# Optimization experiments

Measured on AMD Instinct MI355X. Metric: run time of the kernel, lower is better.

The kernel has to match this reference:

```python
import jax, jax.numpy as jnp
import numpy as np

B, C_CONV, C_TRANS, L = 2048, 64, 64, 16
CT = C_CONV + C_TRANS            # 128 input channels
DIM = C_TRANS                    # transformer width (must equal trans_dim)
HEADS, DIM_HEAD = 8, 64          # Attention defaults
INNER = HEADS * DIM_HEAD         # 512
DEPTH, FF_HID = 2, 256           # Block1D -> Transformer defaults
WLEN = 4                         # Attention.lenth (hardcoded in source)
SCALE = DIM_HEAD ** -0.5

# static relative-position indices (16x16) from 4x4 coordinate grid
_cord = np.array([[i, j] for i in range(WLEN) for j in range(WLEN)])
_rel = _cord[:, None, :] - _cord[None, :, :] + WLEN - 1   # values in [0, 6]
_REL0, _REL1 = _rel[..., 0], _rel[..., 1]

def _build_sw_mask():
    h, w, p, shift = HEADS // 2, 2, WLEN, WLEN // 2
    m = np.zeros((h, w, p, p, p, p), dtype=bool)
    s = p - shift
    m[-1, :, :s, :, s:, :] = True
    m[-1, :, s:, :, :s, :] = True
    m[:, -1, :, :s, :, s:] = True
    m[:, -1, :, s:, :, :s] = True
    return jnp.asarray(m.reshape(1, h * w, p * p, p * p))  # (1, heads, 16, 16)

_MASK = _build_sw_mask()

def _ln(x, g, b, eps=1e-5):
    m = x.mean(-1, keepdims=True)
    v = ((x - m) ** 2).mean(-1, keepdims=True)
    return (x - m) / jnp.sqrt(v + eps) * g + b

def _conv1d(x, w, b, pad):
    y = jax.lax.conv_general_dilated(x, w, (1,), [(pad, pad)],
                                     dimension_numbers=('NCH', 'OIH', 'NCH'))
    return y + b[None, :, None]

def _attention(x, qkv_w, qkv_b, proj_w, proj_b, relpos):
    b, n, _ = x.shape
    x = jnp.roll(x, -(n // 2), axis=1)            # SW cyclic shift (never un-rolled, as in source)
    qkv = x @ qkv_w.T + qkv_b                     # (b, n, 3*inner)
    q, k, v = jnp.split(qkv, 3, axis=-1)
    sh = lambda t: t.reshape(b, n, HEADS, DIM_HEAD).transpose(0, 2, 1, 3)
    q, k, v = sh(q), sh(k), sh(v)
    dots = jnp.einsum('bhid,bhjd->bhij', q, k) * SCALE
    dots = dots + relpos[:, _REL0, _REL1][None]   # gathered relative-position bias (heads,n,n)
    dots = jnp.where(_MASK[:, :, :n, :n], -1e9, dots)
    attn = jax.nn.softmax(dots, axis=-1)
    out = jnp.einsum('bhij,bhjd->bhid', attn, v)
    out = out.transpose(0, 2, 1, 3).reshape(b, n, INNER)
    return out @ proj_w.T + proj_b

def _forward(x, c11_w, c11_b, c12_w, c12_b, lse1_w, lse1_b, lse2_w, lse2_b,
             ln1_g, ln1_b, ln2_g, ln2_b, mlp1_w, mlp1_b, mlp2_w, mlp2_b,
             aln_g, aln_b, qkv_w, qkv_b, proj_w, proj_b, relpos,
             fln_g, fln_b, ff1_w, ff1_b, ff2_w, ff2_b):
    y = jax.nn.relu(_conv1d(x, c11_w, c11_b, 0))
    conv_x, trans_x = y[:, :C_CONV], y[:, C_CONV:]
    # LSE residual block, plus the extra residual in VSE.forward
    t = jax.nn.leaky_relu(_conv1d(conv_x, lse1_w, lse1_b, 1), 0.01)
    t = jax.nn.leaky_relu(_conv1d(t, lse2_w, lse2_b, 1), 0.01)
    conv_x = (t + conv_x) + conv_x
    # GSE: Block1D(trans_dim, trans_dim, dim)
    h = trans_x.transpose(0, 2, 1)                # (b, l, c)
    z = _ln(h, ln1_g, ln1_b)
    for i in range(DEPTH):
        z = _attention(_ln(z, aln_g[i], aln_b[i]), qkv_w[i], qkv_b[i],
                       proj_w[i], proj_b[i], relpos[i]) + z
        f = _ln(z, fln_g[i], fln_b[i])
        f = jax.nn.gelu(f @ ff1_w[i].T + ff1_b[i], approximate=False)
        z = f @ ff2_w[i].T + ff2_b[i] + z
    h = h + z                                     # x + msa(ln1(x))
    m = _ln(h, ln2_g, ln2_b)
    m = jax.nn.gelu(m @ mlp1_w.T + mlp1_b, approximate=False)
    h = h + (m @ mlp2_w.T + mlp2_b)               # x + mlp(ln2(x))
    trans_out = h.transpose(0, 2, 1)              # (b, c, l)
    res = _conv1d(jnp.concatenate([conv_x, trans_out], axis=1), c12_w, c12_b, 0)
    return x + res

def setup_inputs() -> dict:
    key = jax.random.key(0)
    ks = iter(jax.random.split(key, 40))
    rnd = lambda shape, s=0.02: jax.random.normal(next(ks), shape, jnp.float32) * s
    return {
        'x': jax.random.normal(next(ks), (B, CT, L), jnp.float32),
        'c11_w': rnd((CT, CT, 1), 0.05), 'c11_b': rnd((CT,)),
        'c12_w': rnd((CT, CT, 1), 0.05), 'c12_b': rnd((CT,)),
        'lse1_w': rnd((C_CONV, C_CONV, 3), 0.05), 'lse1_b': rnd((C_CONV,)),
        'lse2_w': rnd((C_CONV, C_CONV, 3), 0.05), 'lse2_b': rnd((C_CONV,)),
        'ln1_g': jnp.ones((DIM,)), 'ln1_b': jnp.zeros((DIM,)),
        'ln2_g': jnp.ones((DIM,)), 'ln2_b': jnp.zeros((DIM,)),
        'mlp1_w': rnd((4 * DIM, DIM)), 'mlp1_b': rnd((4 * DIM,)),
        'mlp2_w': rnd((DIM, 4 * DIM)), 'mlp2_b': rnd((DIM,)),
        'aln_g': jnp.ones((DEPTH, DIM)), 'aln_b': jnp.zeros((DEPTH, DIM)),
        'qkv_w': rnd((DEPTH, 3 * INNER, DIM)), 'qkv_b': rnd((DEPTH, 3 * INNER)),
        'proj_w': rnd((DEPTH, DIM, INNER)), 'proj_b': rnd((DEPTH, DIM)),
        'relpos': rnd((DEPTH, HEADS, 2 * WLEN - 1, 2 * WLEN - 1)),
        'fln_g': jnp.ones((DEPTH, DIM)), 'fln_b': jnp.zeros((DEPTH, DIM)),
        'ff1_w': rnd((DEPTH, FF_HID, DIM)), 'ff1_b': rnd((DEPTH, FF_HID)),
        'ff2_w': rnd((DEPTH, DIM, FF_HID)), 'ff2_b': rnd((DEPTH, DIM)),
    }

def reference(x, c11_w, c11_b, c12_w, c12_b, lse1_w, lse1_b, lse2_w, lse2_b,
              ln1_g, ln1_b, ln2_g, ln2_b, mlp1_w, mlp1_b, mlp2_w, mlp2_b,
              aln_g, aln_b, qkv_w, qkv_b, proj_w, proj_b, relpos,
              fln_g, fln_b, ff1_w, ff1_b, ff2_w, ff2_b):
    return _forward(x, c11_w, c11_b, c12_w, c12_b, lse1_w, lse1_b, lse2_w, lse2_b,
                    ln1_g, ln1_b, ln2_g, ln2_b, mlp1_w, mlp1_b, mlp2_w, mlp2_b,
                    aln_g, aln_b, qkv_w, qkv_b, proj_w, proj_b, relpos,
                    fln_g, fln_b, ff1_w, ff1_b, ff2_w, ff2_b)
```

## Files before the change

### kernel.cpp

```cpp
#include <hip/hip_runtime.h>
#include <math.h>

#define SA 68
#define SX 132

__device__ __forceinline__ float lrelu_f(float v){ return v > 0.f ? v : 0.01f*v; }
__device__ __forceinline__ float gelu_f(float v){ return 0.5f*v*(1.f + erff(v*0.70710678118654752f)); }

template<int ND, int K, int WS, int IS, int OS, int UNR>
__device__ __forceinline__ void gemm_nd(const float* __restrict__ in,
                                        const float* __restrict__ W,
                                        const float* __restrict__ bias,
                                        float* __restrict__ outp,
                                        int tid, int act, bool accum)
{
    const int l  = tid & 15;
    const int dq = tid >> 4;
    float acc[ND][4];
#pragma unroll
    for (int nb = 0; nb < ND; ++nb)
#pragma unroll
        for (int dd = 0; dd < 4; ++dd) acc[nb][dd] = 0.f;
    const float* inrow = in + l*IS;
    const float* wbase = W + (size_t)dq*4*WS;
#pragma unroll 1
    for (int k0 = 0; k0 < K; k0 += UNR*4) {
#pragma unroll
        for (int u = 0; u < UNR; ++u) {
            const int k = k0 + u*4;
            const float4 a4 = *(const float4*)(inrow + k);
#pragma unroll
            for (int nb = 0; nb < ND; ++nb) {
#pragma unroll
                for (int dd = 0; dd < 4; ++dd) {
                    const float4 w4 = *(const float4*)(wbase + (size_t)(nb*64 + dd)*WS + k);
                    acc[nb][dd] += w4.x*a4.x + w4.y*a4.y + w4.z*a4.z + w4.w*a4.w;
                }
            }
        }
    }
#pragma unroll
    for (int nb = 0; nb < ND; ++nb)
#pragma unroll
        for (int dd = 0; dd < 4; ++dd) {
            const int d = nb*64 + dq*4 + dd;
            float v = acc[nb][dd] + (bias ? bias[d] : 0.f);
            if (act == 1) v = v > 0.f ? v : 0.f;
            else if (act == 2) v = gelu_f(v);
            float* o = outp + l*OS + d;
            if (accum) *o += v; else *o = v;
        }
}

__device__ __forceinline__ void ln16x64(const float* __restrict__ in,
                                        float* __restrict__ outb,
                                        const float* __restrict__ g, const float* __restrict__ bvec,
                                        int tid, bool roll)
{
    const int r = tid >> 4, c0 = (tid & 15) * 4;
    const float4 v = *(const float4*)(in + r*SA + c0);
    float s  = v.x + v.y + v.z + v.w;
    float sq = v.x*v.x + v.y*v.y + v.z*v.z + v.w*v.w;
#pragma unroll
    for (int m = 1; m < 16; m <<= 1) { s += __shfl_xor(s, m, 64); sq += __shfl_xor(sq, m, 64); }
    const float mean = s * (1.f/64.f);
    const float var  = sq * (1.f/64.f) - mean*mean;
    const float rstd = rsqrtf(var + 1e-5f);
    const int rd = roll ? ((r + 8) & 15) : r;
    const float4 gv = *(const float4*)(g + c0);
    const float4 bv = *(const float4*)(bvec + c0);
    float4 o;
    o.x = (v.x-mean)*rstd*gv.x + bv.x;
    o.y = (v.y-mean)*rstd*gv.y + bv.y;
    o.z = (v.z-mean)*rstd*gv.z + bv.z;
    o.w = (v.w-mean)*rstd*gv.w + bv.w;
    *(float4*)(outb + rd*SA + c0) = o;
}

__device__ __forceinline__ void conv3_lrelu(const float* __restrict__ in,
                                            float* __restrict__ outb,
                                            const float* __restrict__ w, const float* __restrict__ bias,
                                            int tid, int mode, float* __restrict__ cxbuf)
{
    const int o = tid >> 2, l0 = (tid & 3) * 4;
    float acc[4] = {0.f, 0.f, 0.f, 0.f};
    const float* wr0 = w + (size_t)o*64*3;
#pragma unroll 4
    for (int i = 0; i < 64; ++i) {
        const float* wr = wr0 + i*3;
        const float w0 = wr[0], w1 = wr[1], w2 = wr[2];
        const float* row = in + i*16 + l0;
        const float xm1 = (l0 == 0)  ? 0.f : row[-1];
        const float x0 = row[0], x1 = row[1], x2 = row[2], x3 = row[3];
        const float xp1 = (l0 == 12) ? 0.f : row[4];
        acc[0] += w0*xm1 + w1*x0 + w2*x1;
        acc[1] += w0*x0  + w1*x1 + w2*x2;
        acc[2] += w0*x1  + w1*x2 + w2*x3;
        acc[3] += w0*x2  + w1*x3 + w2*xp1;
    }
    const float bb = bias[o];
    if (mode == 0) {
#pragma unroll
        for (int j = 0; j < 4; ++j) outb[o*16 + l0 + j] = lrelu_f(acc[j] + bb);
    } else {
#pragma unroll
        for (int j = 0; j < 4; ++j) {
            float* p = cxbuf + o*16 + l0 + j;
            *p = lrelu_f(acc[j] + bb) + 2.f * (*p);
        }
    }
}

__global__ __launch_bounds__(256)
__attribute__((amdgpu_waves_per_eu(4, 4)))
void vse_fused(
    const float* __restrict__ x,
    const float* __restrict__ c11_w, const float* __restrict__ c11_b,
    const float* __restrict__ c12_w, const float* __restrict__ c12_b,
    const float* __restrict__ lse1_w, const float* __restrict__ lse1_b,
    const float* __restrict__ lse2_w, const float* __restrict__ lse2_b,
    const float* __restrict__ ln1_g, const float* __restrict__ ln1_b,
    const float* __restrict__ ln2_g, const float* __restrict__ ln2_b,
    const float* __restrict__ mlp1_w, const float* __restrict__ mlp1_b,
    const float* __restrict__ mlp2_w, const float* __restrict__ mlp2_b,
    const float* __restrict__ aln_g, const float* __restrict__ aln_b,
    const float* __restrict__ qkv_w, const float* __restrict__ qkv_b,
    const float* __restrict__ proj_w, const float* __restrict__ proj_b,
    const float* __restrict__ relpos,
    const float* __restrict__ fln_g, const float* __restrict__ fln_b,
    const float* __restrict__ ff1_w, const float* __restrict__ ff1_b,
    const float* __restrict__ ff2_w, const float* __restrict__ ff2_b,
    float* __restrict__ out)
{
    __shared__ float pool[9664];
    float* const s_h   = pool;
    float* const s_z   = pool + 1088;
    float* const s_a   = pool + 2176;
    float* const s_q   = pool + 3264;
    float* const s_k   = pool + 4352;
    float* const s_v   = pool + 5440;
    float* const s_fh  = pool + 6528;
    float* const s_cx  = pool + 8640;
    float* const s_xt  = s_q;
    float* const s_y   = s_fh;
    float* const s_t1  = s_a;
    float* const s_o   = s_fh;
    float* const s_att = s_fh + 1088;
    float* const s_cat = s_q;
    float* const s_res = s_fh;

    const int tid = threadIdx.x;
    const int b = blockIdx.x;
    const float* xb = x + (size_t)b * 2048;

#pragma unroll
    for (int it = 0; it < 8; ++it) {
        const int idx = tid + it*256;
        const int c = idx >> 4, l = idx & 15;
        s_xt[l*SX + c] = xb[idx];
    }
    __syncthreads();

    gemm_nd<2,128,128,SX,SX,2>(s_xt, c11_w, c11_b, s_y, tid, 1, false);
    __syncthreads();

#pragma unroll
    for (int it = 0; it < 4; ++it) {
        const int idx = tid + it*256;
        const int i = idx & 63, l = idx >> 6;
        s_cx[i*16 + l] = s_y[l*SX + i];
        s_h [l*SA + i] = s_y[l*SX + 64 + i];
    }
    __syncthreads();

    conv3_lrelu(s_cx, s_t1, lse1_w, lse1_b, tid, 0, nullptr);
    __syncthreads();
    conv3_lrelu(s_t1, nullptr, lse2_w, lse2_b, tid, 1, s_cx);
    __syncthreads();

    ln16x64(s_h, s_z, ln1_g, ln1_b, tid, false);
    __syncthreads();

    for (int layer = 0; layer < 2; ++layer) {
        const float* qkv_wl  = qkv_w + (size_t)layer * 1536 * 64;
        const float* qkv_bl  = qkv_b + layer * 1536;
        const float* proj_wl = proj_w + (size_t)layer * 64 * 512;
        const float* proj_bl = proj_b + layer * 64;
        const float* rel_l   = relpos + layer * 8 * 49;

        ln16x64(s_z, s_a, aln_g + layer*64, aln_b + layer*64, tid, true);
        __syncthreads();

        for (int hh = 0; hh < 8; ++hh) {
            gemm_nd<1,64,64,SA,SA,4>(s_a, qkv_wl + (size_t)(hh*64)*64,        qkv_bl + hh*64,        s_q, tid, 0, false);
            gemm_nd<1,64,64,SA,SA,4>(s_a, qkv_wl + (size_t)(512 + hh*64)*64,  qkv_bl + 512 + hh*64,  s_k, tid, 0, false);
            gemm_nd<1,64,64,SA,SA,4>(s_a, qkv_wl + (size_t)(1024 + hh*64)*64, qkv_bl + 1024 + hh*64, s_v, tid, 0, false);
            __syncthreads();

            {
                const int i = tid >> 4, j = tid & 15;
                const float* qi = s_q + i*SA;
                const float* kj = s_k + j*SA;
                float dot = 0.f;
#pragma unroll 4
                for (int d0 = 0; d0 < 64; d0 += 4) {
                    const float4 qv = *(const float4*)(qi + d0);
                    const float4 kv = *(const float4*)(kj + d0);
                    dot += qv.x*kv.x + qv.y*kv.y + qv.z*kv.z + qv.w*kv.w;
                }
                float val = dot * 0.125f
                          + rel_l[hh*49 + ((i>>2) - (j>>2) + 3)*7 + ((i&3) - (j&3) + 3)];
                const bool masked = ((hh >= 6) && (((i>>2) < 2) != ((j>>2) < 2)))
                                 || ((hh & 1) && (((i&3) < 2) != ((j&3) < 2)));
                if (masked) val = -1e9f;
                float mx = val;
#pragma unroll
                for (int m = 1; m < 16; m <<= 1) mx = fmaxf(mx, __shfl_xor(mx, m, 64));
                const float e = expf(val - mx);
                float ssum = e;
#pragma unroll
                for (int m = 1; m < 16; m <<= 1) ssum += __shfl_xor(ssum, m, 64);
                s_att[i*16 + j] = e / ssum;
            }
            __syncthreads();

            {
                const int l = tid & 15, dq = tid >> 4;
                float a0 = 0.f, a1 = 0.f, a2 = 0.f, a3 = 0.f;
#pragma unroll 4
                for (int j = 0; j < 16; ++j) {
                    const float at = s_att[l*16 + j];
                    const float4 v4 = *(const float4*)(s_v + j*SA + dq*4);
                    a0 += at*v4.x; a1 += at*v4.y; a2 += at*v4.z; a3 += at*v4.w;
                }
                float* op = s_o + l*SA + dq*4;
                op[0] = a0; op[1] = a1; op[2] = a2; op[3] = a3;
            }
            __syncthreads();

            gemm_nd<1,64,512,SA,SA,4>(s_o, proj_wl + hh*64,
                                      (hh == 0) ? proj_bl : nullptr, s_z, tid, 0, true);
            __syncthreads();
        }

        ln16x64(s_z, s_a, fln_g + layer*64, fln_b + layer*64, tid, false);
        __syncthreads();
#pragma unroll
        for (int p = 0; p < 2; ++p) {
            gemm_nd<2,64,64,SA,SX,2>(s_a, ff1_w + (size_t)layer*256*64 + (size_t)p*128*64,
                                     ff1_b + layer*256 + p*128, s_fh, tid, 2, false);
            __syncthreads();
            gemm_nd<1,128,256,SX,SA,4>(s_fh, ff2_w + (size_t)layer*64*256 + p*128,
                                       (p == 0) ? (ff2_b + layer*64) : nullptr, s_z, tid, 0, true);
            __syncthreads();
        }
    }

#pragma unroll
    for (int it = 0; it < 4; ++it) {
        const int idx = tid + it*256;
        const int d = idx & 63, l = idx >> 6;
        s_h[l*SA + d] += s_z[l*SA + d];
    }
    __syncthreads();
    ln16x64(s_h, s_a, ln2_g, ln2_b, tid, false);
    __syncthreads();
#pragma unroll
    for (int p = 0; p < 2; ++p) {
        gemm_nd<2,64,64,SA,SX,2>(s_a, mlp1_w + (size_t)p*128*64, mlp1_b + p*128, s_fh, tid, 2, false);
        __syncthreads();
        gemm_nd<1,128,256,SX,SA,4>(s_fh, mlp2_w + p*128,
                                   (p == 0) ? mlp2_b : nullptr, s_h, tid, 0, true);
        __syncthreads();
    }

#pragma unroll
    for (int it = 0; it < 8; ++it) {
        const int idx = tid + it*256;
        const int i = idx & 127, l = idx >> 7;
        s_cat[l*SX + i] = (i < 64) ? s_cx[i*16 + l] : s_h[l*SA + (i - 64)];
    }
    __syncthreads();

    gemm_nd<2,128,128,SX,SX,2>(s_cat, c12_w, c12_b, s_res, tid, 0, false);
    __syncthreads();

    float* ob = out + (size_t)b * 2048;
#pragma unroll
    for (int it = 0; it < 8; ++it) {
        const int idx = tid + it*256;
        const int c = idx >> 4, l = idx & 15;
        ob[idx] = xb[idx] + s_res[l*SX + c];
    }
}

extern "C" void kernel_launch(void* const* d_in, const int* in_sizes, int n_in,
                              void* d_out, int out_size, void* d_ws, size_t ws_size,
                              hipStream_t stream)
{
    const float* x      = (const float*)d_in[0];
    const float* c11_w  = (const float*)d_in[1];
    const float* c11_b  = (const float*)d_in[2];
    const float* c12_w  = (const float*)d_in[3];
    const float* c12_b  = (const float*)d_in[4];
    const float* lse1_w = (const float*)d_in[5];
    const float* lse1_b = (const float*)d_in[6];
    const float* lse2_w = (const float*)d_in[7];
    const float* lse2_b = (const float*)d_in[8];
    const float* ln1_g  = (const float*)d_in[9];
    const float* ln1_b  = (const float*)d_in[10];
    const float* ln2_g  = (const float*)d_in[11];
    const float* ln2_b  = (const float*)d_in[12];
    const float* mlp1_w = (const float*)d_in[13];
    const float* mlp1_b = (const float*)d_in[14];
    const float* mlp2_w = (const float*)d_in[15];
    const float* mlp2_b = (const float*)d_in[16];
    const float* aln_g  = (const float*)d_in[17];
    const float* aln_b  = (const float*)d_in[18];
    const float* qkv_w  = (const float*)d_in[19];
    const float* qkv_b  = (const float*)d_in[20];
    const float* proj_w = (const float*)d_in[21];
    const float* proj_b = (const float*)d_in[22];
    const float* relpos = (const float*)d_in[23];
    const float* fln_g  = (const float*)d_in[24];
    const float* fln_b  = (const float*)d_in[25];
    const float* ff1_w  = (const float*)d_in[26];
    const float* ff1_b  = (const float*)d_in[27];
    const float* ff2_w  = (const float*)d_in[28];
    const float* ff2_b  = (const float*)d_in[29];

    const int B = in_sizes[0] / (128 * 16);

    vse_fused<<<dim3(B), dim3(256), 0, stream>>>(
        x, c11_w, c11_b, c12_w, c12_b, lse1_w, lse1_b, lse2_w, lse2_b,
        ln1_g, ln1_b, ln2_g, ln2_b, mlp1_w, mlp1_b, mlp2_w, mlp2_b,
        aln_g, aln_b, qkv_w, qkv_b, proj_w, proj_b, relpos,
        fln_g, fln_b, ff1_w, ff1_b, ff2_w, ff2_b,
        (float*)d_out);
}
```

Measured before the change: 1.477 ms.

## Assign one attention head per wavefront with wave-local sync and reduced projection

Attention now runs with each of the four wavefronts handling its own head, in two passes, instead of all 256 threads walking the eight heads in turn. Each wave keeps private q/k/v/attention buffers in LDS and synchronizes with an lgkmcnt wait rather than block barriers. The per-head output projections are written to separate buffers and summed across waves into the residual. This removes most block-wide barriers per head, but shared memory roughly doubles and the waves_per_eu occupancy hint is dropped, which may reduce occupancy.

```diff
diff --git a/kernel.cpp b/kernel.cpp
--- a/kernel.cpp
+++ b/kernel.cpp
@@ -3,9 +3,21 @@
 
 #define SA 68
 #define SX 132
+#define SW 66
+
+#define P_H   0
+#define P_Z   1088
+#define P_A   2176
+#define P_FH  3264
+#define P_CX  5376
+#define P_WQ  6400
+#define P_WK  10624
+#define P_WV  14848
+#define POOLF 19072
 
 __device__ __forceinline__ float lrelu_f(float v){ return v > 0.f ? v : 0.01f*v; }
 __device__ __forceinline__ float gelu_f(float v){ return 0.5f*v*(1.f + erff(v*0.70710678118654752f)); }
+__device__ __forceinline__ void wave_sync(){ asm volatile("s_waitcnt lgkmcnt(0)" ::: "memory"); }
 
 template<int ND, int K, int WS, int IS, int OS, int UNR>
 __device__ __forceinline__ void gemm_nd(const float* __restrict__ in,
@@ -50,6 +62,36 @@
             float* o = outp + l*OS + d;
             if (accum) *o += v; else *o = v;
         }
+}
+
+template<int WS>
+__device__ __forceinline__ void wgemm64(const float* __restrict__ arow,
+                                        const float* __restrict__ wb,
+                                        const float* __restrict__ bb,
+                                        float* __restrict__ outrow, int dq)
+{
+#pragma unroll
+    for (int cq = 0; cq < 4; ++cq) {
+        float acc[4] = {0.f, 0.f, 0.f, 0.f};
+#pragma unroll 1
+        for (int k0 = 0; k0 < 64; k0 += 8) {
+#pragma unroll
+            for (int u = 0; u < 2; ++u) {
+                const int k = k0 + u*4;
+                const float4 a4 = *(const float4*)(arow + k);
+#pragma unroll
+                for (int dd = 0; dd < 4; ++dd) {
+                    const float4 w4 = *(const float4*)(wb + (size_t)(cq*16 + dq*4 + dd)*WS + k);
+                    acc[dd] += w4.x*a4.x + w4.y*a4.y + w4.z*a4.z + w4.w*a4.w;
+                }
+            }
+        }
+#pragma unroll
+        for (int dd = 0; dd < 4; ++dd) {
+            const int c = cq*16 + dq*4 + dd;
+            outrow[c] = acc[dd] + (bb ? bb[c] : 0.f);
+        }
+    }
 }
 
 __device__ __forceinline__ void ln16x64(const float* __restrict__ in,
@@ -111,9 +153,7 @@
     }
 }
 
-__global__ __launch_bounds__(256)
-__attribute__((amdgpu_waves_per_eu(4, 4)))
-void vse_fused(
+__global__ __launch_bounds__(256) void vse_fused(
     const float* __restrict__ x,
     const float* __restrict__ c11_w, const float* __restrict__ c11_b,
     const float* __restrict__ c12_w, const float* __restrict__ c12_b,
@@ -132,26 +172,28 @@
     const float* __restrict__ ff2_w, const float* __restrict__ ff2_b,
     float* __restrict__ out)
 {
-    __shared__ float pool[9664];
-    float* const s_h   = pool;
-    float* const s_z   = pool + 1088;
-    float* const s_a   = pool + 2176;
-    float* const s_q   = pool + 3264;
-    float* const s_k   = pool + 4352;
-    float* const s_v   = pool + 5440;
-    float* const s_fh  = pool + 6528;
-    float* const s_cx  = pool + 8640;
-    float* const s_xt  = s_q;
+    __shared__ float pool[POOLF];
+    float* const s_h   = pool + P_H;
+    float* const s_z   = pool + P_Z;
+    float* const s_a   = pool + P_A;
+    float* const s_fh  = pool + P_FH;
+    float* const s_cx  = pool + P_CX;
+    float* const s_xt  = pool + P_WQ;
     float* const s_y   = s_fh;
     float* const s_t1  = s_a;
-    float* const s_o   = s_fh;
-    float* const s_att = s_fh + 1088;
-    float* const s_cat = s_q;
+    float* const s_cat = pool + P_WQ;
     float* const s_res = s_fh;
 
-    const int tid = threadIdx.x;
+    const int tid  = threadIdx.x;
+    const int lane = tid & 63;
+    const int wv   = tid >> 6;
     const int b = blockIdx.x;
     const float* xb = x + (size_t)b * 2048;
+
+    float* const wq  = pool + P_WQ + wv*1056;
+    float* const wk  = pool + P_WK + wv*1056;
+    float* const wvv = pool + P_WV + wv*1056;
+    float* const watt = s_fh + wv*272;
 
 #pragma unroll
     for (int it = 0; it < 8; ++it) {
@@ -182,64 +224,102 @@
     __syncthreads();
 
     for (int layer = 0; layer < 2; ++layer) {
-        const float* qkv_wl  = qkv_w + (size_t)layer * 1536 * 64;
+        const float* qkv_wl  = qkv_w + (size_t)layer * 98304;
         const float* qkv_bl  = qkv_b + layer * 1536;
-        const float* proj_wl = proj_w + (size_t)layer * 64 * 512;
+        const float* proj_wl = proj_w + (size_t)layer * 32768;
         const float* proj_bl = proj_b + layer * 64;
         const float* rel_l   = relpos + layer * 8 * 49;
 
         ln16x64(s_z, s_a, aln_g + layer*64, aln_b + layer*64, tid, true);
         __syncthreads();
 
-        for (int hh = 0; hh < 8; ++hh) {
-            gemm_nd<1,64,64,SA,SA,4>(s_a, qkv_wl + (size_t)(hh*64)*64,        qkv_bl + hh*64,        s_q, tid, 0, false);
-            gemm_nd<1,64,64,SA,SA,4>(s_a, qkv_wl + (size_t)(512 + hh*64)*64,  qkv_bl + 512 + hh*64,  s_k, tid, 0, false);
-            gemm_nd<1,64,64,SA,SA,4>(s_a, qkv_wl + (size_t)(1024 + hh*64)*64, qkv_bl + 1024 + hh*64, s_v, tid, 0, false);
-            __syncthreads();
+        const int l  = lane & 15;
+        const int dq = lane >> 4;
+        for (int pass = 0; pass < 2; ++pass) {
+            const int hh = pass*4 + wv;
+
+            const float* arow = s_a + l*SA;
+            wgemm64<64>(arow, qkv_wl + (size_t)(hh*64)*64,          qkv_bl + hh*64,          wq  + l*SW, dq);
+            wgemm64<64>(arow, qkv_wl + (size_t)(512 + hh*64)*64,    qkv_bl + 512 + hh*64,    wk  + l*SW, dq);
+            wgemm64<64>(arow, qkv_wl + (size_t)(1024 + hh*64)*64,   qkv_bl + 1024 + hh*64,   wvv + l*SW, dq);
+            wave_sync();
 
             {
-                const int i = tid >> 4, j = tid & 15;
-                const float* qi = s_q + i*SA;
-                const float* kj = s_k + j*SA;
-                float dot = 0.f;
+                const int j = lane & 15, i4 = lane >> 4;
+                float att_r[4];
+#pragma unroll
+                for (int r = 0; r < 4; ++r) {
+                    const int i = i4*4 + r;
+                    const float* qi = wq + i*SW;
+                    const float* kj = wk + j*SW;
+                    float dot = 0.f;
 #pragma unroll 4
-                for (int d0 = 0; d0 < 64; d0 += 4) {
-                    const float4 qv = *(const float4*)(qi + d0);
-                    const float4 kv = *(const float4*)(kj + d0);
-                    dot += qv.x*kv.x + qv.y*kv.y + qv.z*kv.z + qv.w*kv.w;
-                }
-                float val = dot * 0.125f
-                          + rel_l[hh*49 + ((i>>2) - (j>>2) + 3)*7 + ((i&3) - (j&3) + 3)];
-                const bool masked = ((hh >= 6) && (((i>>2) < 2) != ((j>>2) < 2)))
-                                 || ((hh & 1) && (((i&3) < 2) != ((j&3) < 2)));
-                if (masked) val = -1e9f;
-                float mx = val;
-#pragma unroll
-                for (int m = 1; m < 16; m <<= 1) mx = fmaxf(mx, __shfl_xor(mx, m, 64));
-                const float e = expf(val - mx);
-                float ssum = e;
-#pragma unroll
-                for (int m = 1; m < 16; m <<= 1) ssum += __shfl_xor(ssum, m, 64);
-                s_att[i*16 + j] = e / ssum;
+                    for (int d0 = 0; d0 < 64; d0 += 4) {
+                        const float4 qv = *(const float4*)(qi + d0);
+                        const float4 kv = *(const float4*)(kj + d0);
+                        dot += qv.x*kv.x + qv.y*kv.y + qv.z*kv.z + qv.w*kv.w;
+                    }
+                    float val = dot * 0.125f
+                              + rel_l[hh*49 + ((i>>2) - (j>>2) + 3)*7 + ((i&3) - (j&3) + 3)];
+                    const bool masked = ((hh >= 6) && (((i>>2) < 2) != ((j>>2) < 2)))
+                                     || ((hh & 1) && (((i&3) < 2) != ((j&3) < 2)));
+                    if (masked) val = -1e9f;
+                    att_r[r] = val;
+                }
+#pragma unroll
+                for (int r = 0; r < 4; ++r) {
+                    float mx = att_r[r];
+#pragma unroll
+                    for (int m = 1; m < 16; m <<= 1) mx = fmaxf(mx, __shfl_xor(mx, m, 64));
+                    const float e = expf(att_r[r] - mx);
+                    float ssum = e;
+#pragma unroll
+                    for (int m = 1; m < 16; m <<= 1) ssum += __shfl_xor(ssum, m, 64);
+                    watt[(i4*4 + r)*17 + j] = e / ssum;
+                }
             }
-            __syncthreads();
+            wave_sync();
 
             {
-                const int l = tid & 15, dq = tid >> 4;
-                float a0 = 0.f, a1 = 0.f, a2 = 0.f, a3 = 0.f;
+                float o16[4][4];
+#pragma unroll
+                for (int cq = 0; cq < 4; ++cq)
+#pragma unroll
+                    for (int dd = 0; dd < 4; ++dd) o16[cq][dd] = 0.f;
 #pragma unroll 4
                 for (int j = 0; j < 16; ++j) {
-                    const float at = s_att[l*16 + j];
-                    const float4 v4 = *(const float4*)(s_v + j*SA + dq*4);
-                    a0 += at*v4.x; a1 += at*v4.y; a2 += at*v4.z; a3 += at*v4.w;
-                }
-                float* op = s_o + l*SA + dq*4;
-                op[0] = a0; op[1] = a1; op[2] = a2; op[3] = a3;
+                    const float at = watt[l*17 + j];
+                    const float* vr = wvv + j*SW + dq*4;
+#pragma unroll
+                    for (int cq = 0; cq < 4; ++cq) {
+                        const float4 v4 = *(const float4*)(vr + cq*16);
+                        o16[cq][0] += at*v4.x; o16[cq][1] += at*v4.y;
+                        o16[cq][2] += at*v4.z; o16[cq][3] += at*v4.w;
+                    }
+                }
+                wave_sync();
+#pragma unroll
+                for (int cq = 0; cq < 4; ++cq) {
+                    float4 o4; o4.x = o16[cq][0]; o4.y = o16[cq][1]; o4.z = o16[cq][2]; o4.w = o16[cq][3];
+                    *(float4*)(wk + l*SW + cq*16 + dq*4) = o4;
+                }
             }
+            wave_sync();
+
+            wgemm64<512>(wk + l*SW, proj_wl + hh*64, nullptr, wq + l*SW, dq);
+
             __syncthreads();
-
-            gemm_nd<1,64,512,SA,SA,4>(s_o, proj_wl + hh*64,
-                                      (hh == 0) ? proj_bl : nullptr, s_z, tid, 0, true);
+#pragma unroll
+            for (int it = 0; it < 4; ++it) {
+                const int idx = tid + it*256;
+                const int lr = idx >> 6, d = idx & 63;
+                float s = pool[P_WQ + 0*1056 + lr*SW + d]
+                        + pool[P_WQ + 1*1056 + lr*SW + d]
+                        + pool[P_WQ + 2*1056 + lr*SW + d]
+                        + pool[P_WQ + 3*1056 + lr*SW + d];
+                if (pass == 0) s += proj_bl[d];
+                s_z[lr*SA + d] += s;
+            }
             __syncthreads();
         }
 
```

Result: slower. 1.803 ms (+22.1%).

## Remap GEMM threads to output columns and batch per-head projection into one GEMM

Applied to the files above, without the earlier changes.

The per-thread GEMM mapping changes from one row with four columns to four rows with one column. Each thread now reads a single weight row once and reuses it across four rows held in LDS. This makes the global weight loads coalesced across lanes instead of strided, and lowers weight traffic per block. The per-head attention outputs are gathered into a 16x512 LDS buffer so the output projection runs as a single K=512 GEMM after all heads, removing eight accumulate passes and their barriers. LDS use roughly doubles (about 73KB) and launch bounds change to request 2 blocks per CU, which may reduce occupancy.

```diff
diff --git a/kernel.cpp b/kernel.cpp
--- a/kernel.cpp
+++ b/kernel.cpp
@@ -3,53 +3,72 @@
 
 #define SA 68
 #define SX 132
+#define SO 520
+
+#define P_H   0
+#define P_Z   1088
+#define P_A   2176
+#define P_FH  3264
+#define P_CX  5376
+#define P_Q   6400
+#define P_K   7488
+#define P_V   8576
+#define P_OA  9664
+#define P_ATT 17984
+#define POOLF 18256
 
 __device__ __forceinline__ float lrelu_f(float v){ return v > 0.f ? v : 0.01f*v; }
 __device__ __forceinline__ float gelu_f(float v){ return 0.5f*v*(1.f + erff(v*0.70710678118654752f)); }
 
-template<int ND, int K, int WS, int IS, int OS, int UNR>
-__device__ __forceinline__ void gemm_nd(const float* __restrict__ in,
+template<int NB, int K, int WS, int IS, int OS, int UNR>
+__device__ __forceinline__ void gemm_rc(const float* __restrict__ in,
                                         const float* __restrict__ W,
                                         const float* __restrict__ bias,
                                         float* __restrict__ outp,
                                         int tid, int act, bool accum)
 {
-    const int l  = tid & 15;
-    const int dq = tid >> 4;
-    float acc[ND][4];
-#pragma unroll
-    for (int nb = 0; nb < ND; ++nb)
-#pragma unroll
-        for (int dd = 0; dd < 4; ++dd) acc[nb][dd] = 0.f;
-    const float* inrow = in + l*IS;
-    const float* wbase = W + (size_t)dq*4*WS;
+    const int rg = tid >> 6;
+    const int c0 = tid & 63;
+    float acc[NB][4];
+#pragma unroll
+    for (int nb = 0; nb < NB; ++nb)
+#pragma unroll
+        for (int i = 0; i < 4; ++i) acc[nb][i] = 0.f;
+    const float* inb = in + rg*4*IS;
 #pragma unroll 1
     for (int k0 = 0; k0 < K; k0 += UNR*4) {
 #pragma unroll
         for (int u = 0; u < UNR; ++u) {
             const int k = k0 + u*4;
-            const float4 a4 = *(const float4*)(inrow + k);
-#pragma unroll
-            for (int nb = 0; nb < ND; ++nb) {
-#pragma unroll
-                for (int dd = 0; dd < 4; ++dd) {
-                    const float4 w4 = *(const float4*)(wbase + (size_t)(nb*64 + dd)*WS + k);
-                    acc[nb][dd] += w4.x*a4.x + w4.y*a4.y + w4.z*a4.z + w4.w*a4.w;
-                }
-            }
-        }
-    }
-#pragma unroll
-    for (int nb = 0; nb < ND; ++nb)
-#pragma unroll
-        for (int dd = 0; dd < 4; ++dd) {
-            const int d = nb*64 + dq*4 + dd;
-            float v = acc[nb][dd] + (bias ? bias[d] : 0.f);
-            if (act == 1) v = v > 0.f ? v : 0.f;
+            float4 w4[NB];
+#pragma unroll
+            for (int nb = 0; nb < NB; ++nb)
+                w4[nb] = *(const float4*)(W + (size_t)(nb*64 + c0)*WS + k);
+            float4 a4[4];
+#pragma unroll
+            for (int i = 0; i < 4; ++i)
+                a4[i] = *(const float4*)(inb + i*IS + k);
+#pragma unroll
+            for (int nb = 0; nb < NB; ++nb)
+#pragma unroll
+                for (int i = 0; i < 4; ++i)
+                    acc[nb][i] += a4[i].x*w4[nb].x + a4[i].y*w4[nb].y
+                                + a4[i].z*w4[nb].z + a4[i].w*w4[nb].w;
+        }
+    }
+#pragma unroll
+    for (int nb = 0; nb < NB; ++nb) {
+        const int c = nb*64 + c0;
+        const float bv = bias ? bias[c] : 0.f;
+#pragma unroll
+        for (int i = 0; i < 4; ++i) {
+            float v = acc[nb][i] + bv;
+            if (act == 1) v = fmaxf(v, 0.f);
             else if (act == 2) v = gelu_f(v);
-            float* o = outp + l*OS + d;
+            float* o = outp + (rg*4 + i)*OS + c;
             if (accum) *o += v; else *o = v;
         }
+    }
 }
 
 __device__ __forceinline__ void ln16x64(const float* __restrict__ in,
@@ -111,9 +130,7 @@
     }
 }
 
-__global__ __launch_bounds__(256)
-__attribute__((amdgpu_waves_per_eu(4, 4)))
-void vse_fused(
+__global__ __launch_bounds__(256, 2) void vse_fused(
     const float* __restrict__ x,
     const float* __restrict__ c11_w, const float* __restrict__ c11_b,
     const float* __restrict__ c12_w, const float* __restrict__ c12_b,
@@ -132,20 +149,20 @@
     const float* __restrict__ ff2_w, const float* __restrict__ ff2_b,
     float* __restrict__ out)
 {
-    __shared__ float pool[9664];
-    float* const s_h   = pool;
-    float* const s_z   = pool + 1088;
-    float* const s_a   = pool + 2176;
-    float* const s_q   = pool + 3264;
-    float* const s_k   = pool + 4352;
-    float* const s_v   = pool + 5440;
-    float* const s_fh  = pool + 6528;
-    float* const s_cx  = pool + 8640;
+    __shared__ float pool[POOLF];
+    float* const s_h   = pool + P_H;
+    float* const s_z   = pool + P_Z;
+    float* const s_a   = pool + P_A;
+    float* const s_fh  = pool + P_FH;
+    float* const s_cx  = pool + P_CX;
+    float* const s_q   = pool + P_Q;
+    float* const s_k   = pool + P_K;
+    float* const s_v   = pool + P_V;
+    float* const s_oa  = pool + P_OA;
+    float* const s_att = pool + P_ATT;
     float* const s_xt  = s_q;
     float* const s_y   = s_fh;
     float* const s_t1  = s_a;
-    float* const s_o   = s_fh;
-    float* const s_att = s_fh + 1088;
     float* const s_cat = s_q;
     float* const s_res = s_fh;
 
@@ -161,7 +178,7 @@
     }
     __syncthreads();
 
-    gemm_nd<2,128,128,SX,SX,2>(s_xt, c11_w, c11_b, s_y, tid, 1, false);
+    gemm_rc<2,128,128,SX,SX,4>(s_xt, c11_w, c11_b, s_y, tid, 1, false);
     __syncthreads();
 
 #pragma unroll
@@ -182,9 +199,9 @@
     __syncthreads();
 
     for (int layer = 0; layer < 2; ++layer) {
-        const float* qkv_wl  = qkv_w + (size_t)layer * 1536 * 64;
+        const float* qkv_wl  = qkv_w + (size_t)layer * 98304;
         const float* qkv_bl  = qkv_b + layer * 1536;
-        const float* proj_wl = proj_w + (size_t)layer * 64 * 512;
+        const float* proj_wl = proj_w + (size_t)layer * 32768;
         const float* proj_bl = proj_b + layer * 64;
         const float* rel_l   = relpos + layer * 8 * 49;
 
@@ -192,9 +209,9 @@
         __syncthreads();
 
         for (int hh = 0; hh < 8; ++hh) {
-            gemm_nd<1,64,64,SA,SA,4>(s_a, qkv_wl + (size_t)(hh*64)*64,        qkv_bl + hh*64,        s_q, tid, 0, false);
-            gemm_nd<1,64,64,SA,SA,4>(s_a, qkv_wl + (size_t)(512 + hh*64)*64,  qkv_bl + 512 + hh*64,  s_k, tid, 0, false);
-            gemm_nd<1,64,64,SA,SA,4>(s_a, qkv_wl + (size_t)(1024 + hh*64)*64, qkv_bl + 1024 + hh*64, s_v, tid, 0, false);
+            gemm_rc<1,64,64,SA,SA,8>(s_a, qkv_wl + (size_t)(hh*64)*64,        qkv_bl + hh*64,        s_q, tid, 0, false);
+            gemm_rc<1,64,64,SA,SA,8>(s_a, qkv_wl + (size_t)(512 + hh*64)*64,  qkv_bl + 512 + hh*64,  s_k, tid, 0, false);
+            gemm_rc<1,64,64,SA,SA,8>(s_a, qkv_wl + (size_t)(1024 + hh*64)*64, qkv_bl + 1024 + hh*64, s_v, tid, 0, false);
             __syncthreads();
 
             {
@@ -220,7 +237,7 @@
                 float ssum = e;
 #pragma unroll
                 for (int m = 1; m < 16; m <<= 1) ssum += __shfl_xor(ssum, m, 64);
-                s_att[i*16 + j] = e / ssum;
+                s_att[i*17 + j] = e / ssum;
             }
             __syncthreads();
 
@@ -229,28 +246,27 @@
                 float a0 = 0.f, a1 = 0.f, a2 = 0.f, a3 = 0.f;
 #pragma unroll 4
                 for (int j = 0; j < 16; ++j) {
-                    const float at = s_att[l*16 + j];
+                    const float at = s_att[l*17 + j];
                     const float4 v4 = *(const float4*)(s_v + j*SA + dq*4);
                     a0 += at*v4.x; a1 += at*v4.y; a2 += at*v4.z; a3 += at*v4.w;
                 }
-                float* op = s_o + l*SA + dq*4;
+                float* op = s_oa + l*SO + hh*64 + dq*4;
                 op[0] = a0; op[1] = a1; op[2] = a2; op[3] = a3;
             }
             __syncthreads();
-
-            gemm_nd<1,64,512,SA,SA,4>(s_o, proj_wl + hh*64,
-                                      (hh == 0) ? proj_bl : nullptr, s_z, tid, 0, true);
-            __syncthreads();
-        }
+        }
+
+        gemm_rc<1,512,512,SO,SA,8>(s_oa, proj_wl, proj_bl, s_z, tid, 0, true);
+        __syncthreads();
 
         ln16x64(s_z, s_a, fln_g + layer*64, fln_b + layer*64, tid, false);
         __syncthreads();
 #pragma unroll
         for (int p = 0; p < 2; ++p) {
-            gemm_nd<2,64,64,SA,SX,2>(s_a, ff1_w + (size_t)layer*256*64 + (size_t)p*128*64,
+            gemm_rc<2,64,64,SA,SX,4>(s_a, ff1_w + (size_t)layer*256*64 + (size_t)p*128*64,
                                      ff1_b + layer*256 + p*128, s_fh, tid, 2, false);
             __syncthreads();
-            gemm_nd<1,128,256,SX,SA,4>(s_fh, ff2_w + (size_t)layer*64*256 + p*128,
+            gemm_rc<1,128,256,SX,SA,8>(s_fh, ff2_w + (size_t)layer*64*256 + p*128,
                                        (p == 0) ? (ff2_b + layer*64) : nullptr, s_z, tid, 0, true);
             __syncthreads();
         }
@@ -267,9 +283,9 @@
     __syncthreads();
 #pragma unroll
     for (int p = 0; p < 2; ++p) {
-        gemm_nd<2,64,64,SA,SX,2>(s_a, mlp1_w + (size_t)p*128*64, mlp1_b + p*128, s_fh, tid, 2, false);
-        __syncthreads();
-        gemm_nd<1,128,256,SX,SA,4>(s_fh, mlp2_w + p*128,
+        gemm_rc<2,64,64,SA,SX,4>(s_a, mlp1_w + (size_t)p*128*64, mlp1_b + p*128, s_fh, tid, 2, false);
+        __syncthreads();
+        gemm_rc<1,128,256,SX,SA,8>(s_fh, mlp2_w + p*128,
                                    (p == 0) ? mlp2_b : nullptr, s_h, tid, 0, true);
         __syncthreads();
     }
@@ -282,7 +298,7 @@
     }
     __syncthreads();
 
-    gemm_nd<2,128,128,SX,SX,2>(s_cat, c12_w, c12_b, s_res, tid, 0, false);
+    gemm_rc<2,128,128,SX,SX,4>(s_cat, c12_w, c12_b, s_res, tid, 0, false);
     __syncthreads();
 
     float* ob = out + (size_t)b * 2048;
```

Result: slower. 1.550 ms (+4.9%).
